# Kernel tuning notes

Hardware: AMD Instinct MI355X
Metric: run time of the kernel (lower is better)

The kernel has to match this reference:

```python
import jax, jax.numpy as jnp
import numpy as np

FT_IN = 40960
VFT_IN = 640


def _sparse_linear(indices, values, W, b, B):
    # y[r] = sum_{k: row[k]==r} values[k] * W[:, col[k]]  + b
    # W: [out, in]; gather columns as rows of W.T -> [nnz, out]
    rows = indices[0]
    cols = indices[1]
    contrib = W.T[cols] * values[:, None]          # [nnz, out]
    acc = jnp.zeros((B, W.shape[0]), dtype=W.dtype).at[rows].add(contrib)
    return acc + b


def setup_inputs() -> dict:
    B = 8192
    NNZ_PER_POS = 32
    NNZ = B * NNZ_PER_POS
    FT_OUT = 256
    key = jax.random.key(0)
    ks = jax.random.split(key, 8)

    def make_indices(k):
        kb, kf = jax.random.split(k)
        bids = jax.random.randint(kb, (NNZ,), 0, B, dtype=jnp.int32)
        fids = jax.random.randint(kf, (NNZ,), 0, FT_IN, dtype=jnp.int32)
        return jnp.stack([bids, fids], axis=0)  # [2, NNZ]

    s = 1.0 / np.sqrt(FT_IN)
    sv = 1.0 / np.sqrt(VFT_IN)
    so = 1.0 / np.sqrt(2 * FT_OUT)
    return {
        "stm_indices": make_indices(ks[0]),
        "nstm_indices": make_indices(ks[1]),
        "values": jnp.ones((NNZ,), dtype=jnp.float32),
        "size": B,
        "ft_w": jax.random.uniform(ks[2], (FT_OUT, FT_IN), jnp.float32, -s, s),
        "ft_b": jax.random.uniform(ks[3], (FT_OUT,), jnp.float32, -s, s),
        "fft_w": jax.random.uniform(ks[4], (FT_OUT, VFT_IN), jnp.float32, -sv, sv),
        "fft_b": jax.random.uniform(ks[5], (FT_OUT,), jnp.float32, -sv, sv),
        "out_w": jax.random.uniform(ks[6], (1, 2 * FT_OUT), jnp.float32, -so, so),
        "out_b": jax.random.uniform(ks[7], (1,), jnp.float32, -so, so),
    }


def reference(stm_indices, nstm_indices, values, size, ft_w, ft_b, fft_w, fft_b, out_w, out_b):
    B = size
    # factorized (virtual) feature indices: column % 640
    v_stm = jnp.stack([stm_indices[0], stm_indices[1] % VFT_IN], axis=0)
    v_nstm = jnp.stack([nstm_indices[0], nstm_indices[1] % VFT_IN], axis=0)

    stm_ft = _sparse_linear(stm_indices, values, ft_w, ft_b, B) + \
             _sparse_linear(v_stm, values, fft_w, fft_b, B) - fft_b  # bias added once in torch? no:
    # NOTE: torch adds both biases (ft.bias and fft.bias); undo the subtraction above.
    stm_ft = stm_ft + fft_b
    nstm_ft = _sparse_linear(nstm_indices, values, ft_w, ft_b, B) + \
              _sparse_linear(v_nstm, values, fft_w, fft_b, B)

    hidden = jnp.clip(jnp.concatenate([stm_ft, nstm_ft], axis=1), 0.0, 1.0)  # [B, 2*ft_out]
    return jax.nn.sigmoid(hidden @ out_w.T + out_b)  # [B, 1]
```

## Files before the change

kernel.cpp:

```cpp
#include <hip/hip_runtime.h>
#include <math.h>

#define FT_OUT 256
#define VFT 640
#define CAP 96

typedef _Float16 half8_t __attribute__((ext_vector_type(8)));
typedef float    float8_t __attribute__((ext_vector_type(8)));

__global__ __launch_bounds__(256) void prep_k(
    const float* __restrict__ ft_w, const float* __restrict__ fft_w,
    _Float16* __restrict__ W2h, int ft_in,
    const int* __restrict__ stm, const int* __restrict__ nstm,
    const float* __restrict__ vals, int nnz,
    int* __restrict__ cnt_s, int* __restrict__ cnt_n,
    int2* __restrict__ slot_s, int2* __restrict__ slot_n, int nfill)
{
    __shared__ float tile[64][65];
    __shared__ float ftile[64][65];
    if ((int)blockIdx.x < nfill) {
        int k = (int)blockIdx.x * 256 + threadIdx.x;
        if (k >= nnz) return;
        int vb = __float_as_int(vals[k]);
        int r = stm[k], c = stm[nnz + k];
        int pos = atomicAdd(&cnt_s[r], 1);
        if (pos < CAP) slot_s[(size_t)r * CAP + pos] = make_int2(c, vb);
        r = nstm[k]; c = nstm[nnz + k];
        pos = atomicAdd(&cnt_n[r], 1);
        if (pos < CAP) slot_n[(size_t)r * CAP + pos] = make_int2(c, vb);
    } else {
        int bx = (int)blockIdx.x - nfill;
        int cb = (bx >> 2) * 64;
        int ob = (bx & 3) * 64;
        int fvb = cb % VFT;
        int tc4 = threadIdx.x & 15, tr = threadIdx.x >> 4;
#pragma unroll
        for (int i = 0; i < 4; i++) {
            int o = i * 16 + tr;
            const float4 f = *(const float4*)(ft_w + (size_t)(ob + o) * ft_in + cb + tc4 * 4);
            const float4 g = *(const float4*)(fft_w + (size_t)(ob + o) * VFT + fvb + tc4 * 4);
            tile[o][tc4 * 4 + 0] = f.x; tile[o][tc4 * 4 + 1] = f.y;
            tile[o][tc4 * 4 + 2] = f.z; tile[o][tc4 * 4 + 3] = f.w;
            ftile[o][tc4 * 4 + 0] = g.x; ftile[o][tc4 * 4 + 1] = g.y;
            ftile[o][tc4 * 4 + 2] = g.z; ftile[o][tc4 * 4 + 3] = g.w;
        }
        __syncthreads();
        int g = threadIdx.x & 7, cl = threadIdx.x >> 3;
#pragma unroll
        for (int i = 0; i < 2; i++) {
            int c = i * 32 + cl, col = cb + c;
            half8_t h;
#pragma unroll
            for (int jj = 0; jj < 8; jj++)
                h[jj] = (_Float16)(tile[g * 8 + jj][c] + ftile[g * 8 + jj][c]);
            *(half8_t*)(W2h + (size_t)col * FT_OUT + ob + g * 8) = h;
        }
    }
}

__global__ __launch_bounds__(256) void fused_k(const _Float16* __restrict__ W2h,
    const int* __restrict__ cnt_s, const int2* __restrict__ slot_s,
    const int* __restrict__ cnt_n, const int2* __restrict__ slot_n,
    const float* __restrict__ ft_b, const float* __restrict__ fft_b,
    const float* __restrict__ out_w, const float* __restrict__ out_b,
    float* __restrict__ out, int B) {
    int lane = threadIdx.x & 63;
    int wid  = threadIdx.x >> 6;
    int row  = blockIdx.x * 2 + (wid >> 1);
    int side = wid & 1;
    int hi   = lane >> 5;
    int sl   = lane & 31;

    const int*  cnt  = side ? cnt_n : cnt_s;
    const int2* slot = (side ? slot_n : slot_s) + (size_t)row * CAP;
    int n = min(cnt[row], CAP);

    float8_t acc;
#pragma unroll
    for (int k = 0; k < 8; k++) acc[k] = 0.f;
    if (hi == 0) {
        const float4* fb = (const float4*)(ft_b + sl * 8);
        const float4* gb = (const float4*)(fft_b + sl * 8);
        float4 a0 = fb[0], a1 = fb[1], c0 = gb[0], c1 = gb[1];
        acc[0] = a0.x + c0.x; acc[1] = a0.y + c0.y; acc[2] = a0.z + c0.z; acc[3] = a0.w + c0.w;
        acc[4] = a1.x + c1.x; acc[5] = a1.y + c1.y; acc[6] = a1.z + c1.z; acc[7] = a1.w + c1.w;
    }

#define PROC(e)                                                                     \
    {                                                                               \
        int   c_ = hi ? (e).z : (e).x;                                              \
        float v_ = __int_as_float(hi ? (e).w : (e).y);                              \
        const half8_t w_ = *(const half8_t*)(W2h + ((size_t)c_ << 8) + (sl << 3));  \
        _Pragma("unroll")                                                           \
        for (int k = 0; k < 8; k++) acc[k] += v_ * (float)w_[k];                    \
    }

    int j = 0;
    for (; j + 8 <= n; j += 8) {
        const int4 e0 = *(const int4*)(slot + j);
        const int4 e1 = *(const int4*)(slot + j + 2);
        const int4 e2 = *(const int4*)(slot + j + 4);
        const int4 e3 = *(const int4*)(slot + j + 6);
        PROC(e0) PROC(e1) PROC(e2) PROC(e3)
    }
    for (; j + 2 <= n; j += 2) {
        const int4 e = *(const int4*)(slot + j);
        PROC(e)
    }
    if (j < n) {
        const int2 e = slot[j];
        int   c_ = hi ? 0 : e.x;
        float v_ = hi ? 0.f : __int_as_float(e.y);
        const half8_t w_ = *(const half8_t*)(W2h + ((size_t)c_ << 8) + (sl << 3));
#pragma unroll
        for (int k = 0; k < 8; k++) acc[k] += v_ * (float)w_[k];
    }
#undef PROC

#pragma unroll
    for (int k = 0; k < 8; k++) {
        float o = __shfl_xor(acc[k], 32, 64);
        acc[k] = fminf(fmaxf(acc[k] + o, 0.f), 1.f);
    }

    const float4* ow = (const float4*)(out_w + side * FT_OUT + sl * 8);
    const float4 w0 = ow[0], w1 = ow[1];
    float p = acc[0] * w0.x + acc[1] * w0.y + acc[2] * w0.z + acc[3] * w0.w
            + acc[4] * w1.x + acc[5] * w1.y + acc[6] * w1.z + acc[7] * w1.w;
#pragma unroll
    for (int m = 32; m >= 1; m >>= 1) p += __shfl_xor(p, m, 64);
    p *= 0.5f;

    __shared__ float part[4];
    if (lane == 0) part[wid] = p;
    __syncthreads();
    if (threadIdx.x < 2) {
        float q = part[threadIdx.x * 2] + part[threadIdx.x * 2 + 1] + out_b[0];
        out[blockIdx.x * 2 + threadIdx.x] = 1.f / (1.f + __expf(-q));
    }
}

extern "C" void kernel_launch(void* const* d_in, const int* in_sizes, int n_in,
                              void* d_out, int out_size, void* d_ws, size_t ws_size,
                              hipStream_t stream) {
    const int*   stm    = (const int*)d_in[0];
    const int*   nstm   = (const int*)d_in[1];
    const float* values = (const float*)d_in[2];
    const float* ft_w   = (const float*)d_in[4];
    const float* ft_b   = (const float*)d_in[5];
    const float* fft_w  = (const float*)d_in[6];
    const float* fft_b  = (const float*)d_in[7];
    const float* out_w  = (const float*)d_in[8];
    const float* out_b  = (const float*)d_in[9];
    float* out = (float*)d_out;

    int B = out_size;
    int nnz = in_sizes[0] / 2;
    int ft_in = in_sizes[4] / FT_OUT;

    _Float16* W2h  = (_Float16*)d_ws;
    int2*  slot_s  = (int2*)(W2h + (size_t)ft_in * FT_OUT);
    int2*  slot_n  = slot_s + (size_t)B * CAP;
    int*   cnt_s   = (int*)(slot_n + (size_t)B * CAP);
    int*   cnt_n   = cnt_s + B;

    int nbuild = (ft_in / 64) * (FT_OUT / 64);
    int nfill  = (nnz + 255) / 256;

    hipMemsetAsync(cnt_s, 0, 2 * (size_t)B * sizeof(int), stream);
    prep_k<<<nfill + nbuild, 256, 0, stream>>>(ft_w, fft_w, W2h, ft_in,
                                               stm, nstm, values, nnz,
                                               cnt_s, cnt_n, slot_s, slot_n, nfill);
    fused_k<<<B / 2, 256, 0, stream>>>(W2h, cnt_s, slot_s, cnt_n, slot_n,
                                       ft_b, fft_b, out_w, out_b, out, B);
}
```

Measured before the change: 163.2 us.

## Slice fused weight table by output columns and split gather across slice blocks

The fused fp16 weight table is re-laid out as eight 32-column slices, so each gather block touches only one slice (40960×32 halves) and gets a smaller, cache-friendly working set. The gather kernel now runs one block per (row group, slice), accumulates partial output dot-products and combines them with float atomics into a per-row accumulator. A separate sigmoid kernel applies the bias and activation. The prep kernel also splits the stm/nstm fill work into separate blocks and pre-sums the two weight tiles in shared memory. The cost is more total blocks, redundant slot-list reads across the eight slices, atomics, and an extra kernel launch.

```diff
diff --git a/kernel.cpp b/kernel.cpp
--- a/kernel.cpp
+++ b/kernel.cpp
@@ -4,140 +4,124 @@
 #define FT_OUT 256
 #define VFT 640
 #define CAP 96
+#define SLICE 32
+#define NSLICE 8
 
 typedef _Float16 half8_t __attribute__((ext_vector_type(8)));
-typedef float    float8_t __attribute__((ext_vector_type(8)));
+typedef _Float16 half2_t __attribute__((ext_vector_type(2)));
 
 __global__ __launch_bounds__(256) void prep_k(
     const float* __restrict__ ft_w, const float* __restrict__ fft_w,
-    _Float16* __restrict__ W2h, int ft_in,
+    _Float16* __restrict__ W2s, int ft_in,
     const int* __restrict__ stm, const int* __restrict__ nstm,
     const float* __restrict__ vals, int nnz,
     int* __restrict__ cnt_s, int* __restrict__ cnt_n,
     int2* __restrict__ slot_s, int2* __restrict__ slot_n, int nfill)
 {
+    int bx = (int)blockIdx.x;
+    if (bx < nfill) {
+        int side = bx & 1;
+        int k = (bx >> 1) * 256 + threadIdx.x;
+        if (k >= nnz) return;
+        const int* src = side ? nstm : stm;
+        int* cnt = side ? cnt_n : cnt_s;
+        int2* slotb = side ? slot_n : slot_s;
+        int r = src[k], c = src[nnz + k];
+        int vb = __float_as_int(vals[k]);
+        int pos = atomicAdd(&cnt[r], 1);
+        if (pos < CAP) slotb[(size_t)r * CAP + pos] = make_int2(c, vb);
+        return;
+    }
     __shared__ float tile[64][65];
-    __shared__ float ftile[64][65];
-    if ((int)blockIdx.x < nfill) {
-        int k = (int)blockIdx.x * 256 + threadIdx.x;
-        if (k >= nnz) return;
-        int vb = __float_as_int(vals[k]);
-        int r = stm[k], c = stm[nnz + k];
-        int pos = atomicAdd(&cnt_s[r], 1);
-        if (pos < CAP) slot_s[(size_t)r * CAP + pos] = make_int2(c, vb);
-        r = nstm[k]; c = nstm[nnz + k];
-        pos = atomicAdd(&cnt_n[r], 1);
-        if (pos < CAP) slot_n[(size_t)r * CAP + pos] = make_int2(c, vb);
-    } else {
-        int bx = (int)blockIdx.x - nfill;
-        int cb = (bx >> 2) * 64;
-        int ob = (bx & 3) * 64;
-        int fvb = cb % VFT;
-        int tc4 = threadIdx.x & 15, tr = threadIdx.x >> 4;
+    bx -= nfill;
+    int cb = (bx >> 2) * 64;
+    int ob = (bx & 3) * 64;
+    int fvb = cb % VFT;
+    int tc4 = threadIdx.x & 15, tr = threadIdx.x >> 4;
 #pragma unroll
-        for (int i = 0; i < 4; i++) {
-            int o = i * 16 + tr;
-            const float4 f = *(const float4*)(ft_w + (size_t)(ob + o) * ft_in + cb + tc4 * 4);
-            const float4 g = *(const float4*)(fft_w + (size_t)(ob + o) * VFT + fvb + tc4 * 4);
-            tile[o][tc4 * 4 + 0] = f.x; tile[o][tc4 * 4 + 1] = f.y;
-            tile[o][tc4 * 4 + 2] = f.z; tile[o][tc4 * 4 + 3] = f.w;
-            ftile[o][tc4 * 4 + 0] = g.x; ftile[o][tc4 * 4 + 1] = g.y;
-            ftile[o][tc4 * 4 + 2] = g.z; ftile[o][tc4 * 4 + 3] = g.w;
-        }
-        __syncthreads();
-        int g = threadIdx.x & 7, cl = threadIdx.x >> 3;
+    for (int i = 0; i < 4; i++) {
+        int o = i * 16 + tr;
+        const float4 f = *(const float4*)(ft_w + (size_t)(ob + o) * ft_in + cb + tc4 * 4);
+        const float4 g = *(const float4*)(fft_w + (size_t)(ob + o) * VFT + fvb + tc4 * 4);
+        tile[o][tc4 * 4 + 0] = f.x + g.x; tile[o][tc4 * 4 + 1] = f.y + g.y;
+        tile[o][tc4 * 4 + 2] = f.z + g.z; tile[o][tc4 * 4 + 3] = f.w + g.w;
+    }
+    __syncthreads();
+    int g = threadIdx.x & 7, cl = threadIdx.x >> 3;
 #pragma unroll
-        for (int i = 0; i < 2; i++) {
-            int c = i * 32 + cl, col = cb + c;
-            half8_t h;
+    for (int i = 0; i < 2; i++) {
+        int c = i * 32 + cl, col = cb + c;
+        int obase = ob + g * 8;
+        int slice = obase >> 5, sub = obase & 31;
+        half8_t h;
 #pragma unroll
-            for (int jj = 0; jj < 8; jj++)
-                h[jj] = (_Float16)(tile[g * 8 + jj][c] + ftile[g * 8 + jj][c]);
-            *(half8_t*)(W2h + (size_t)col * FT_OUT + ob + g * 8) = h;
-        }
+        for (int jj = 0; jj < 8; jj++) h[jj] = (_Float16)tile[g * 8 + jj][c];
+        *(half8_t*)(W2s + (((size_t)(slice * ft_in + col)) << 5) + sub) = h;
     }
 }
 
-__global__ __launch_bounds__(256) void fused_k(const _Float16* __restrict__ W2h,
+__global__ __launch_bounds__(256) void gather_k(
+    const _Float16* __restrict__ W2s,
     const int* __restrict__ cnt_s, const int2* __restrict__ slot_s,
     const int* __restrict__ cnt_n, const int2* __restrict__ slot_n,
     const float* __restrict__ ft_b, const float* __restrict__ fft_b,
-    const float* __restrict__ out_w, const float* __restrict__ out_b,
-    float* __restrict__ out, int B) {
-    int lane = threadIdx.x & 63;
-    int wid  = threadIdx.x >> 6;
-    int row  = blockIdx.x * 2 + (wid >> 1);
-    int side = wid & 1;
-    int hi   = lane >> 5;
-    int sl   = lane & 31;
+    const float* __restrict__ out_w, float* __restrict__ racc, int ft_in)
+{
+    int slice = blockIdx.x & 7;
+    int grp   = blockIdx.x >> 3;
+    int wid   = threadIdx.x >> 6;
+    int lane  = threadIdx.x & 63;
+    int row   = grp * 4 + wid;
+    int ent   = lane >> 4;
+    int oo    = (lane & 15) * 2;
+    const _Float16* Wt = W2s + (((size_t)slice * ft_in) << 5) + oo;
+    int og = slice * SLICE + oo;
+    const float2 bias2 = make_float2(ft_b[og] + fft_b[og], ft_b[og + 1] + fft_b[og + 1]);
 
-    const int*  cnt  = side ? cnt_n : cnt_s;
-    const int2* slot = (side ? slot_n : slot_s) + (size_t)row * CAP;
-    int n = min(cnt[row], CAP);
+    float wsum = 0.f;
+#pragma unroll
+    for (int side = 0; side < 2; side++) {
+        const int*  cnt  = side ? cnt_n : cnt_s;
+        const int2* slot = (side ? slot_n : slot_s) + (size_t)row * CAP;
+        int n = min(cnt[row], CAP);
+        float a0 = (ent == 0) ? bias2.x : 0.f;
+        float a1 = (ent == 0) ? bias2.y : 0.f;
+        int steps = (n + 3) >> 2;
+        int s = 0;
+        for (; s + 2 <= steps; s += 2) {
+            int i0 = s * 4 + ent, i1 = i0 + 4;
+            int2 e0 = slot[i0 < n ? i0 : 0];
+            int2 e1 = slot[i1 < n ? i1 : 0];
+            float v0 = (i0 < n) ? __int_as_float(e0.y) : 0.f;
+            float v1 = (i1 < n) ? __int_as_float(e1.y) : 0.f;
+            const half2_t w0 = *(const half2_t*)(Wt + ((size_t)e0.x << 5));
+            const half2_t w1 = *(const half2_t*)(Wt + ((size_t)e1.x << 5));
+            a0 += v0 * (float)w0[0]; a1 += v0 * (float)w0[1];
+            a0 += v1 * (float)w1[0]; a1 += v1 * (float)w1[1];
+        }
+        if (s < steps) {
+            int i0 = s * 4 + ent;
+            int2 e0 = slot[i0 < n ? i0 : 0];
+            float v0 = (i0 < n) ? __int_as_float(e0.y) : 0.f;
+            const half2_t w0 = *(const half2_t*)(Wt + ((size_t)e0.x << 5));
+            a0 += v0 * (float)w0[0]; a1 += v0 * (float)w0[1];
+        }
+        a0 += __shfl_xor(a0, 16, 64); a1 += __shfl_xor(a1, 16, 64);
+        a0 += __shfl_xor(a0, 32, 64); a1 += __shfl_xor(a1, 32, 64);
+        a0 = fminf(fmaxf(a0, 0.f), 1.f);
+        a1 = fminf(fmaxf(a1, 0.f), 1.f);
+        const float2 ow = *(const float2*)(out_w + side * FT_OUT + og);
+        wsum += a0 * ow.x + a1 * ow.y;
+    }
+#pragma unroll
+    for (int m = 1; m <= 8; m <<= 1) wsum += __shfl_xor(wsum, m, 64);
+    if (lane == 0) atomicAdd(&racc[row], wsum);
+}
 
-    float8_t acc;
-#pragma unroll
-    for (int k = 0; k < 8; k++) acc[k] = 0.f;
-    if (hi == 0) {
-        const float4* fb = (const float4*)(ft_b + sl * 8);
-        const float4* gb = (const float4*)(fft_b + sl * 8);
-        float4 a0 = fb[0], a1 = fb[1], c0 = gb[0], c1 = gb[1];
-        acc[0] = a0.x + c0.x; acc[1] = a0.y + c0.y; acc[2] = a0.z + c0.z; acc[3] = a0.w + c0.w;
-        acc[4] = a1.x + c1.x; acc[5] = a1.y + c1.y; acc[6] = a1.z + c1.z; acc[7] = a1.w + c1.w;
-    }
-
-#define PROC(e)                                                                     \
-    {                                                                               \
-        int   c_ = hi ? (e).z : (e).x;                                              \
-        float v_ = __int_as_float(hi ? (e).w : (e).y);                              \
-        const half8_t w_ = *(const half8_t*)(W2h + ((size_t)c_ << 8) + (sl << 3));  \
-        _Pragma("unroll")                                                           \
-        for (int k = 0; k < 8; k++) acc[k] += v_ * (float)w_[k];                    \
-    }
-
-    int j = 0;
-    for (; j + 8 <= n; j += 8) {
-        const int4 e0 = *(const int4*)(slot + j);
-        const int4 e1 = *(const int4*)(slot + j + 2);
-        const int4 e2 = *(const int4*)(slot + j + 4);
-        const int4 e3 = *(const int4*)(slot + j + 6);
-        PROC(e0) PROC(e1) PROC(e2) PROC(e3)
-    }
-    for (; j + 2 <= n; j += 2) {
-        const int4 e = *(const int4*)(slot + j);
-        PROC(e)
-    }
-    if (j < n) {
-        const int2 e = slot[j];
-        int   c_ = hi ? 0 : e.x;
-        float v_ = hi ? 0.f : __int_as_float(e.y);
-        const half8_t w_ = *(const half8_t*)(W2h + ((size_t)c_ << 8) + (sl << 3));
-#pragma unroll
-        for (int k = 0; k < 8; k++) acc[k] += v_ * (float)w_[k];
-    }
-#undef PROC
-
-#pragma unroll
-    for (int k = 0; k < 8; k++) {
-        float o = __shfl_xor(acc[k], 32, 64);
-        acc[k] = fminf(fmaxf(acc[k] + o, 0.f), 1.f);
-    }
-
-    const float4* ow = (const float4*)(out_w + side * FT_OUT + sl * 8);
-    const float4 w0 = ow[0], w1 = ow[1];
-    float p = acc[0] * w0.x + acc[1] * w0.y + acc[2] * w0.z + acc[3] * w0.w
-            + acc[4] * w1.x + acc[5] * w1.y + acc[6] * w1.z + acc[7] * w1.w;
-#pragma unroll
-    for (int m = 32; m >= 1; m >>= 1) p += __shfl_xor(p, m, 64);
-    p *= 0.5f;
-
-    __shared__ float part[4];
-    if (lane == 0) part[wid] = p;
-    __syncthreads();
-    if (threadIdx.x < 2) {
-        float q = part[threadIdx.x * 2] + part[threadIdx.x * 2 + 1] + out_b[0];
-        out[blockIdx.x * 2 + threadIdx.x] = 1.f / (1.f + __expf(-q));
-    }
+__global__ void sigmoid_k(const float* __restrict__ racc, const float* __restrict__ out_b,
+                          float* __restrict__ out, int B) {
+    int i = blockIdx.x * 256 + threadIdx.x;
+    if (i < B) out[i] = 1.f / (1.f + __expf(-(racc[i] + out_b[0])));
 }
 
 extern "C" void kernel_launch(void* const* d_in, const int* in_sizes, int n_in,
@@ -158,19 +142,21 @@
     int nnz = in_sizes[0] / 2;
     int ft_in = in_sizes[4] / FT_OUT;
 
-    _Float16* W2h  = (_Float16*)d_ws;
-    int2*  slot_s  = (int2*)(W2h + (size_t)ft_in * FT_OUT);
+    _Float16* W2s  = (_Float16*)d_ws;
+    int2*  slot_s  = (int2*)(W2s + (size_t)ft_in * FT_OUT);
     int2*  slot_n  = slot_s + (size_t)B * CAP;
     int*   cnt_s   = (int*)(slot_n + (size_t)B * CAP);
     int*   cnt_n   = cnt_s + B;
+    float* racc    = (float*)(cnt_n + B);
 
+    int nfill  = 2 * ((nnz + 255) / 256);
     int nbuild = (ft_in / 64) * (FT_OUT / 64);
-    int nfill  = (nnz + 255) / 256;
 
-    hipMemsetAsync(cnt_s, 0, 2 * (size_t)B * sizeof(int), stream);
-    prep_k<<<nfill + nbuild, 256, 0, stream>>>(ft_w, fft_w, W2h, ft_in,
+    hipMemsetAsync(cnt_s, 0, 3 * (size_t)B * sizeof(int), stream);
+    prep_k<<<nfill + nbuild, 256, 0, stream>>>(ft_w, fft_w, W2s, ft_in,
                                                stm, nstm, values, nnz,
                                                cnt_s, cnt_n, slot_s, slot_n, nfill);
-    fused_k<<<B / 2, 256, 0, stream>>>(W2h, cnt_s, slot_s, cnt_n, slot_n,
-                                       ft_b, fft_b, out_w, out_b, out, B);
+    gather_k<<<(B / 4) * NSLICE, 256, 0, stream>>>(W2s, cnt_s, slot_s, cnt_n, slot_n,
+                                                   ft_b, fft_b, out_w, racc, ft_in);
+    sigmoid_k<<<(B + 255) / 256, 256, 0, stream>>>(racc, out_b, out, B);
 }
```

Result: slower. 203.8 us (+24.8%).

## Pad counters, split fill blocks per side, merge weight tiles, nontemporal slot loads

Applied to the files above, without the earlier changes.

The per-row atomic counters are padded to a 16-int stride so atomics on adjacent rows no longer share a cache line. The fill phase now uses separate blocks for the stm and nstm sides. The weight-build path sums ft_w and fft_w before writing a single shared-memory tile, which halves its LDS footprint. The fused kernel reads slot entries with nontemporal 64-bit loads and selects the half-wave's entry itself, at the cost of a larger counter memset and more counter memory.

```diff
diff --git a/kernel.cpp b/kernel.cpp
--- a/kernel.cpp
+++ b/kernel.cpp
@@ -4,6 +4,7 @@
 #define FT_OUT 256
 #define VFT 640
 #define CAP 96
+#define CPAD 16
 
 typedef _Float16 half8_t __attribute__((ext_vector_type(8)));
 typedef float    float8_t __attribute__((ext_vector_type(8)));
@@ -16,45 +17,43 @@
     int* __restrict__ cnt_s, int* __restrict__ cnt_n,
     int2* __restrict__ slot_s, int2* __restrict__ slot_n, int nfill)
 {
+    int bx = (int)blockIdx.x;
+    if (bx < nfill) {
+        int side = bx & 1;
+        int k = (bx >> 1) * 256 + threadIdx.x;
+        if (k >= nnz) return;
+        const int* src = side ? nstm : stm;
+        int* cnt = side ? cnt_n : cnt_s;
+        int2* slotb = side ? slot_n : slot_s;
+        int r = src[k], c = src[nnz + k];
+        int vb = __float_as_int(vals[k]);
+        int pos = atomicAdd(&cnt[r * CPAD], 1);
+        if (pos < CAP) slotb[(size_t)r * CAP + pos] = make_int2(c, vb);
+        return;
+    }
     __shared__ float tile[64][65];
-    __shared__ float ftile[64][65];
-    if ((int)blockIdx.x < nfill) {
-        int k = (int)blockIdx.x * 256 + threadIdx.x;
-        if (k >= nnz) return;
-        int vb = __float_as_int(vals[k]);
-        int r = stm[k], c = stm[nnz + k];
-        int pos = atomicAdd(&cnt_s[r], 1);
-        if (pos < CAP) slot_s[(size_t)r * CAP + pos] = make_int2(c, vb);
-        r = nstm[k]; c = nstm[nnz + k];
-        pos = atomicAdd(&cnt_n[r], 1);
-        if (pos < CAP) slot_n[(size_t)r * CAP + pos] = make_int2(c, vb);
-    } else {
-        int bx = (int)blockIdx.x - nfill;
-        int cb = (bx >> 2) * 64;
-        int ob = (bx & 3) * 64;
-        int fvb = cb % VFT;
-        int tc4 = threadIdx.x & 15, tr = threadIdx.x >> 4;
+    bx -= nfill;
+    int cb = (bx >> 2) * 64;
+    int ob = (bx & 3) * 64;
+    int fvb = cb % VFT;
+    int tc4 = threadIdx.x & 15, tr = threadIdx.x >> 4;
 #pragma unroll
-        for (int i = 0; i < 4; i++) {
-            int o = i * 16 + tr;
-            const float4 f = *(const float4*)(ft_w + (size_t)(ob + o) * ft_in + cb + tc4 * 4);
-            const float4 g = *(const float4*)(fft_w + (size_t)(ob + o) * VFT + fvb + tc4 * 4);
-            tile[o][tc4 * 4 + 0] = f.x; tile[o][tc4 * 4 + 1] = f.y;
-            tile[o][tc4 * 4 + 2] = f.z; tile[o][tc4 * 4 + 3] = f.w;
-            ftile[o][tc4 * 4 + 0] = g.x; ftile[o][tc4 * 4 + 1] = g.y;
-            ftile[o][tc4 * 4 + 2] = g.z; ftile[o][tc4 * 4 + 3] = g.w;
-        }
-        __syncthreads();
-        int g = threadIdx.x & 7, cl = threadIdx.x >> 3;
+    for (int i = 0; i < 4; i++) {
+        int o = i * 16 + tr;
+        const float4 f = *(const float4*)(ft_w + (size_t)(ob + o) * ft_in + cb + tc4 * 4);
+        const float4 g = *(const float4*)(fft_w + (size_t)(ob + o) * VFT + fvb + tc4 * 4);
+        tile[o][tc4 * 4 + 0] = f.x + g.x; tile[o][tc4 * 4 + 1] = f.y + g.y;
+        tile[o][tc4 * 4 + 2] = f.z + g.z; tile[o][tc4 * 4 + 3] = f.w + g.w;
+    }
+    __syncthreads();
+    int g = threadIdx.x & 7, cl = threadIdx.x >> 3;
 #pragma unroll
-        for (int i = 0; i < 2; i++) {
-            int c = i * 32 + cl, col = cb + c;
-            half8_t h;
+    for (int i = 0; i < 2; i++) {
+        int c = i * 32 + cl, col = cb + c;
+        half8_t h;
 #pragma unroll
-            for (int jj = 0; jj < 8; jj++)
-                h[jj] = (_Float16)(tile[g * 8 + jj][c] + ftile[g * 8 + jj][c]);
-            *(half8_t*)(W2h + (size_t)col * FT_OUT + ob + g * 8) = h;
-        }
+        for (int jj = 0; jj < 8; jj++) h[jj] = (_Float16)tile[g * 8 + jj][c];
+        *(half8_t*)(W2h + (size_t)col * FT_OUT + ob + g * 8) = h;
     }
 }
 
@@ -73,7 +72,7 @@
 
     const int*  cnt  = side ? cnt_n : cnt_s;
     const int2* slot = (side ? slot_n : slot_s) + (size_t)row * CAP;
-    int n = min(cnt[row], CAP);
+    int n = min(cnt[row * CPAD], CAP);
 
     float8_t acc;
 #pragma unroll
@@ -86,36 +85,45 @@
         acc[4] = a1.x + c1.x; acc[5] = a1.y + c1.y; acc[6] = a1.z + c1.z; acc[7] = a1.w + c1.w;
     }
 
-#define PROC(e)                                                                     \
+#define LOADPAIR(j, cc, vv)                                                         \
     {                                                                               \
-        int   c_ = hi ? (e).z : (e).x;                                              \
-        float v_ = __int_as_float(hi ? (e).w : (e).y);                              \
-        const half8_t w_ = *(const half8_t*)(W2h + ((size_t)c_ << 8) + (sl << 3));  \
+        unsigned long long p0 =                                                     \
+            __builtin_nontemporal_load((const unsigned long long*)(slot + (j)));    \
+        unsigned long long p1 =                                                     \
+            __builtin_nontemporal_load((const unsigned long long*)(slot + (j)) + 1);\
+        unsigned long long pe = hi ? p1 : p0;                                       \
+        cc = (int)(pe & 0xffffffffu);                                               \
+        vv = __int_as_float((int)(pe >> 32));                                       \
+    }
+#define PROC(cc, vv)                                                                \
+    {                                                                               \
+        const half8_t w_ = *(const half8_t*)(W2h + ((size_t)(cc) << 8) + (sl << 3));\
         _Pragma("unroll")                                                           \
-        for (int k = 0; k < 8; k++) acc[k] += v_ * (float)w_[k];                    \
+        for (int k = 0; k < 8; k++) acc[k] += (vv) * (float)w_[k];                  \
     }
 
     int j = 0;
     for (; j + 8 <= n; j += 8) {
-        const int4 e0 = *(const int4*)(slot + j);
-        const int4 e1 = *(const int4*)(slot + j + 2);
-        const int4 e2 = *(const int4*)(slot + j + 4);
-        const int4 e3 = *(const int4*)(slot + j + 6);
-        PROC(e0) PROC(e1) PROC(e2) PROC(e3)
+        int c0, c1, c2, c3; float v0, v1, v2, v3;
+        LOADPAIR(j,     c0, v0)
+        LOADPAIR(j + 2, c1, v1)
+        LOADPAIR(j + 4, c2, v2)
+        LOADPAIR(j + 6, c3, v3)
+        PROC(c0, v0) PROC(c1, v1) PROC(c2, v2) PROC(c3, v3)
     }
     for (; j + 2 <= n; j += 2) {
-        const int4 e = *(const int4*)(slot + j);
-        PROC(e)
+        int c0; float v0;
+        LOADPAIR(j, c0, v0)
+        PROC(c0, v0)
     }
     if (j < n) {
         const int2 e = slot[j];
         int   c_ = hi ? 0 : e.x;
         float v_ = hi ? 0.f : __int_as_float(e.y);
-        const half8_t w_ = *(const half8_t*)(W2h + ((size_t)c_ << 8) + (sl << 3));
-#pragma unroll
-        for (int k = 0; k < 8; k++) acc[k] += v_ * (float)w_[k];
+        PROC(c_, v_)
     }
 #undef PROC
+#undef LOADPAIR
 
 #pragma unroll
     for (int k = 0; k < 8; k++) {
@@ -162,12 +170,12 @@
     int2*  slot_s  = (int2*)(W2h + (size_t)ft_in * FT_OUT);
     int2*  slot_n  = slot_s + (size_t)B * CAP;
     int*   cnt_s   = (int*)(slot_n + (size_t)B * CAP);
-    int*   cnt_n   = cnt_s + B;
+    int*   cnt_n   = cnt_s + (size_t)B * CPAD;
 
+    int nfill  = 2 * ((nnz + 255) / 256);
     int nbuild = (ft_in / 64) * (FT_OUT / 64);
-    int nfill  = (nnz + 255) / 256;
 
-    hipMemsetAsync(cnt_s, 0, 2 * (size_t)B * sizeof(int), stream);
+    hipMemsetAsync(cnt_s, 0, 2 * (size_t)B * CPAD * sizeof(int), stream);
     prep_k<<<nfill + nbuild, 256, 0, stream>>>(ft_w, fft_w, W2h, ft_in,
                                                stm, nstm, values, nnz,
                                                cnt_s, cnt_n, slot_s, slot_n, nfill);
```

New measurement: 163.3 us. No clear change (+0.1%).
